# Kernel tuning notes

Hardware: AMD Instinct MI355X
Metric: run time of the kernel (lower is better)

The kernel has to match this reference:

```python
import jax, jax.numpy as jnp
import numpy as np

SEGMENT_LENGTHS = [2048, 4096]
DILATION_RATES = [1, 2]


def _group_attention(qg, kg, vg, seg_len, r, gidx):
    # qg/kg/vg: [b, gh, n, d]; segmented dilated attention for one head group.
    b, gh, n, d = qg.shape
    nseg = n // seg_len
    scale = float(1.0 / np.sqrt(d))
    qs = qg.reshape(b, gh, nseg, seg_len, d)
    ks = kg.reshape(b, gh, nseg, seg_len, d)
    vs = vg.reshape(b, gh, nseg, seg_len, d)
    if r > 1:
        m = seg_len // r
        # offset = (group_idx + seg_idx) % r; pattern = offset + r*arange(m) (no wrap since seg_len % r == 0)
        offsets = (gidx + jnp.arange(nseg)) % r            # [nseg]
        idx = offsets[:, None] + r * jnp.arange(m)[None, :]  # [nseg, m]
        si = jnp.arange(nseg)[:, None]                      # [nseg, 1]
        qd = qs[:, :, si, idx]                              # [b, gh, nseg, m, d]
        kd = ks[:, :, si, idx]
        vd = vs[:, :, si, idx]
    else:
        qd, kd, vd = qs, ks, vs
    scores = jnp.einsum('bgsqd,bgskd->bgsqk', qd, kd) * scale
    attn = jax.nn.softmax(scores, axis=-1)
    out = jnp.einsum('bgsqk,bgskd->bgsqd', attn, vd)
    if r > 1:
        # scatter dilated outputs back to their segment positions; unselected positions stay 0
        full = jnp.zeros((b, gh, nseg, seg_len, d), dtype=qg.dtype)
        out = full.at[:, :, si, idx].set(out)
    return out.reshape(b, gh, n, d)


def reference(q, k, v):
    # q, k, v: [b, n, h, d]; ring_size == 1 -> single-device dilated attention
    b, n, h, d = q.shape
    ngroups = len(SEGMENT_LENGTHS)
    gsize = h // ngroups
    qt = jnp.transpose(q, (0, 2, 1, 3))  # [b, h, n, d]
    kt = jnp.transpose(k, (0, 2, 1, 3))
    vt = jnp.transpose(v, (0, 2, 1, 3))
    outs = []
    for i, (s, r) in enumerate(zip(SEGMENT_LENGTHS, DILATION_RATES)):
        hs, he = i * gsize, (i + 1) * gsize
        outs.append(_group_attention(qt[:, hs:he], kt[:, hs:he], vt[:, hs:he], s, r, i))
    out = jnp.concatenate(outs, axis=1)   # [b, h, n, d]
    return jnp.transpose(out, (0, 2, 1, 3))  # [b, n, h, d]


def setup_inputs() -> dict:
    key = jax.random.key(0)
    kq, kk, kv = jax.random.split(key, 3)
    shape = (1, 8192, 16, 128)
    return {
        'q': jax.random.normal(kq, shape, dtype=jnp.float32),
        'k': jax.random.normal(kk, shape, dtype=jnp.float32),
        'v': jax.random.normal(kv, shape, dtype=jnp.float32),
    }
```

## Files before the change

### kernel.cpp

```cpp
#include <hip/hip_runtime.h>
#include <hip/hip_bf16.h>

typedef __attribute__((ext_vector_type(8)))  short bf16x8;
typedef __attribute__((ext_vector_type(4)))  float f32x4;
typedef __attribute__((ext_vector_type(16))) float f32x16;
typedef __attribute__((ext_vector_type(4)))  int   int4v;

__device__ __forceinline__ short f2bf(float f) {
    unsigned u = __builtin_bit_cast(unsigned, f);
    unsigned r = u + 0x7fffu + ((u >> 16) & 1u);
    return (short)(r >> 16);
}

__device__ __forceinline__ int row_map(int p, int j) {
    if (p < 32) return (p & 3) * 2048 + j;
    return ((p - 32) & 1) == 0 ? (2 * j + 1) : (4096 + 2 * j);
}
__device__ __forceinline__ int head_of(int p) {
    return (p < 32) ? (p >> 2) : (8 + ((p - 32) >> 1));
}

#define GLDS(gsrc, ldst)                                                          \
    __builtin_amdgcn_global_load_lds(                                             \
        (const __attribute__((address_space(1))) unsigned int*)(gsrc),            \
        (__attribute__((address_space(3))) unsigned int*)(ldst), 16, 0, 0)

__global__ __launch_bounds__(256) void conv_k_kernel(
    const float* __restrict__ K, short* __restrict__ Kws)
{
    const int cid = blockIdx.x * 256 + threadIdx.x;
    const int p   = cid >> 15;
    const int rem = cid & 32767;
    const int row = rem >> 4;
    const int d8  = (rem & 15) << 3;
    const int g   = row_map(p, row);
    const float* src = K + ((size_t)(g * 16 + head_of(p))) * 128 + d8;
    bf16x8 o;
    #pragma unroll
    for (int e = 0; e < 8; ++e) o[e] = f2bf(src[e]);
    *(bf16x8*)(Kws + (((size_t)p * 2048 + row) << 7) + d8) = o;
}

__global__ __launch_bounds__(256) void conv_v_kernel(
    const float* __restrict__ V, short* __restrict__ Vws)
{
    __shared__ short T[128][72];
    const int p  = blockIdx.x >> 5;
    const int kb = blockIdx.x & 31;
    const int tid = threadIdx.x;
    const int h = head_of(p);
    #pragma unroll
    for (int it = 0; it < 4; ++it) {
        const int cid  = it * 256 + tid;
        const int krow = cid & 63;
        const int d8   = (cid >> 6) << 3;
        const int g = row_map(p, kb * 64 + krow);
        const float* vp = V + ((size_t)(g * 16 + h)) * 128 + d8;
        #pragma unroll
        for (int e = 0; e < 8; ++e) T[d8 + e][krow] = f2bf(vp[e]);
    }
    __syncthreads();
    #pragma unroll
    for (int it = 0; it < 4; ++it) {
        const int j   = it * 256 + tid;
        const int d   = j >> 3;
        const int c16 = j & 7;
        bf16x8 val = *(const bf16x8*)&T[d][c16 * 8];
        *(bf16x8*)(Vws + ((size_t)p * 128 + d) * 2048 + kb * 64 + c16 * 8) = val;
    }
}

__global__ __launch_bounds__(256, 2) void dilated_attn5_kernel(
    const float* __restrict__ Q, const short* __restrict__ Kws,
    const short* __restrict__ Vws, float* __restrict__ O)
{
    __shared__ short Ks[2][64 * 128];
    __shared__ short Vt[2][128 * 64];
    __shared__ float sbuf[4][32];

    const int logical = (blockIdx.x & 7) * 96 + (blockIdx.x >> 3);
    const int pid  = logical >> 4;
    const int tile = logical & 15;
    const int h    = head_of(pid);

    const int tid  = threadIdx.x;
    const int wave = tid >> 6;
    const int lane = tid & 63;
    const int ql   = lane & 31;
    const int hi   = lane >> 5;

    const float scale_log2e = 0.08838834764831845f * 1.4426950408889634f;

    const short* Kp = Kws + ((size_t)pid * 2048 << 7);
    const short* Vp = Vws + ((size_t)pid * 128) * 2048;

    bf16x8 qf[8];
    {
        const int j = tile * 128 + wave * 32 + ql;
        const int g = row_map(pid, j);
        const float* qp = Q + ((size_t)(g * 16 + h)) * 128 + hi * 8;
        #pragma unroll
        for (int c = 0; c < 8; ++c) {
            bf16x8 f;
            #pragma unroll
            for (int e = 0; e < 8; ++e) f[e] = f2bf(qp[c * 16 + e] * scale_log2e);
            qf[c] = f;
        }
    }

    f32x16 oacc[4];
    #pragma unroll
    for (int dt = 0; dt < 4; ++dt) oacc[dt] = (f32x16)0.f;
    float m = -3.0e38f, l = 0.f;

    auto STAGE = [&](int buf, int kb) {
        #pragma unroll
        for (int it = 0; it < 4; ++it) {
            const int j   = it * 256 + wave * 64 + lane;
            const int row = j >> 4;
            const int u   = j & 15;
            GLDS(Kp + (((size_t)(kb * 64 + row)) << 7) + ((u ^ (row & 15)) << 3),
                 &Ks[buf][(it * 256 + wave * 64) * 8]);
        }
        #pragma unroll
        for (int it = 0; it < 4; ++it) {
            const int j   = it * 256 + wave * 64 + lane;
            const int row = j >> 3;
            const int u   = j & 7;
            GLDS(Vp + (size_t)row * 2048 + kb * 64 + ((u ^ (row & 7)) << 3),
                 &Vt[buf][(it * 256 + wave * 64) * 8]);
        }
    };

    STAGE(0, 0);
    asm volatile("s_waitcnt vmcnt(0)" ::: "memory");
    __syncthreads();

    for (int kb = 0; kb < 32; ++kb) {
        const int cur = kb & 1;
        if (kb + 1 < 32) STAGE(cur ^ 1, kb + 1);

        f32x16 p[2];
        __builtin_amdgcn_s_setprio(1);
        #pragma unroll
        for (int kt2 = 0; kt2 < 2; ++kt2) {
            f32x16 acc = (f32x16)0.f;
            const int row = kt2 * 32 + ql;
            #pragma unroll
            for (int c = 0; c < 8; ++c) {
                const int u = 2 * c + hi;
                bf16x8 a = *(const bf16x8*)&Ks[cur][row * 128 + ((u ^ (row & 15)) << 3)];
                acc = __builtin_amdgcn_mfma_f32_32x32x16_bf16(a, qf[c], acc, 0, 0, 0);
            }
            p[kt2] = acc;
        }
        __builtin_amdgcn_s_setprio(0);

        float rm = p[0][0];
        #pragma unroll
        for (int kt2 = 0; kt2 < 2; ++kt2)
            #pragma unroll
            for (int r = 0; r < 16; ++r) rm = fmaxf(rm, p[kt2][r]);
        rm = fmaxf(rm, __shfl_xor(rm, 32));

        if (__any(rm > m + 8.0f)) {
            const float mn = fmaxf(m, rm);
            const float sf = exp2f(m - mn);
            m = mn;
            l *= sf;
            if (lane < 32) sbuf[wave][lane] = sf;
            #pragma unroll
            for (int r = 0; r < 16; ++r) {
                const float s = sbuf[wave][(r & 3) + 8 * (r >> 2) + 4 * hi];
                #pragma unroll
                for (int dt = 0; dt < 4; ++dt) oacc[dt][r] *= s;
            }
        }

        float rs = 0.f;
        #pragma unroll
        for (int kt2 = 0; kt2 < 2; ++kt2)
            #pragma unroll
            for (int r = 0; r < 16; ++r) {
                const float pv = exp2f(p[kt2][r] - m);
                p[kt2][r] = pv;
                rs += pv;
            }
        rs += __shfl_xor(rs, 32);
        l += rs;

        bf16x8 pa[4];
        #pragma unroll
        for (int kt2 = 0; kt2 < 2; ++kt2) {
            int A0, A1, B0, B1, C0, C1, D0, D1;
            asm("v_cvt_pk_bf16_f32 %0,%1,%2" : "=v"(A0) : "v"(p[kt2][0]),  "v"(p[kt2][1]));
            asm("v_cvt_pk_bf16_f32 %0,%1,%2" : "=v"(A1) : "v"(p[kt2][2]),  "v"(p[kt2][3]));
            asm("v_cvt_pk_bf16_f32 %0,%1,%2" : "=v"(B0) : "v"(p[kt2][4]),  "v"(p[kt2][5]));
            asm("v_cvt_pk_bf16_f32 %0,%1,%2" : "=v"(B1) : "v"(p[kt2][6]),  "v"(p[kt2][7]));
            asm("v_cvt_pk_bf16_f32 %0,%1,%2" : "=v"(C0) : "v"(p[kt2][8]),  "v"(p[kt2][9]));
            asm("v_cvt_pk_bf16_f32 %0,%1,%2" : "=v"(C1) : "v"(p[kt2][10]), "v"(p[kt2][11]));
            asm("v_cvt_pk_bf16_f32 %0,%1,%2" : "=v"(D0) : "v"(p[kt2][12]), "v"(p[kt2][13]));
            asm("v_cvt_pk_bf16_f32 %0,%1,%2" : "=v"(D1) : "v"(p[kt2][14]), "v"(p[kt2][15]));
            asm("v_permlane32_swap_b32 %0, %1" : "+v"(A0), "+v"(B0));
            asm("v_permlane32_swap_b32 %0, %1" : "+v"(A1), "+v"(B1));
            asm("v_permlane32_swap_b32 %0, %1" : "+v"(C0), "+v"(D0));
            asm("v_permlane32_swap_b32 %0, %1" : "+v"(C1), "+v"(D1));
            pa[2 * kt2 + 0] = __builtin_bit_cast(bf16x8, (int4v){A0, A1, B0, B1});
            pa[2 * kt2 + 1] = __builtin_bit_cast(bf16x8, (int4v){C0, C1, D0, D1});
        }

        __builtin_amdgcn_s_setprio(1);
        #pragma unroll
        for (int ks = 0; ks < 4; ++ks) {
            #pragma unroll
            for (int dt = 0; dt < 4; ++dt) {
                const int row = dt * 32 + ql;
                const int u   = 2 * ks + hi;
                bf16x8 vb = *(const bf16x8*)&Vt[cur][row * 64 + ((u ^ (row & 7)) << 3)];
                oacc[dt] = __builtin_amdgcn_mfma_f32_32x32x16_bf16(pa[ks], vb, oacc[dt], 0, 0, 0);
            }
        }
        __builtin_amdgcn_s_setprio(0);

        asm volatile("s_waitcnt vmcnt(0)" ::: "memory");
        __syncthreads();
    }

    if (lane < 32) sbuf[wave][lane] = 1.f / l;
    #pragma unroll
    for (int r = 0; r < 16; ++r) {
        const int qrow = (r & 3) + 8 * (r >> 2) + 4 * hi;
        const float inv = sbuf[wave][qrow];
        const int j = tile * 128 + wave * 32 + qrow;
        const int g = row_map(pid, j);
        float* op = O + ((size_t)(g * 16 + h)) * 128 + ql;
        #pragma unroll
        for (int dt = 0; dt < 4; ++dt)
            op[dt * 32] = oacc[dt][r] * inv;
    }
}

__global__ __launch_bounds__(256) void zero_fill_kernel(float* __restrict__ O)
{
    const int t = blockIdx.x * 256 + threadIdx.x;
    const int c4   = t & 31;
    const int rowi = (t >> 5) & 4095;
    const int hh   = t >> 17;
    const int row  = (rowi < 2048) ? (2 * rowi) : (4096 + 2 * (rowi - 2048) + 1);
    float4 z; z.x = 0.f; z.y = 0.f; z.z = 0.f; z.w = 0.f;
    *(float4*)&O[((size_t)(row * 16) + 8 + hh) * 128 + c4 * 4] = z;
}

#define BK    64
#define KPAD  136
#define VPAD  72
__global__ __launch_bounds__(256) void dilated_attn_v1_kernel(
    const float* __restrict__ Q, const float* __restrict__ K,
    const float* __restrict__ V, float* __restrict__ O)
{
    __shared__ short KsL[BK][KPAD];
    __shared__ short VtL[128][VPAD];
    __shared__ short PsL[4][16][VPAD];
    const int bid  = blockIdx.x;
    const int p    = bid >> 5;
    const int tile = bid & 31;
    const int h    = head_of(p);
    const int tid  = threadIdx.x;
    const int wave = tid >> 6;
    const int lane = tid & 63;
    const int lr   = lane & 15;
    const int lg   = lane >> 4;
    const float scale_log2e = 0.08838834764831845f * 1.4426950408889634f;
    bf16x8 qf[4];
    {
        const int j = tile * 64 + wave * 16 + lr;
        const int g = row_map(p, j);
        const float* qp = Q + ((size_t)(g * 16 + h)) * 128 + lg * 8;
        #pragma unroll
        for (int c = 0; c < 4; ++c) {
            bf16x8 f;
            #pragma unroll
            for (int e = 0; e < 8; ++e) f[e] = f2bf(qp[c * 32 + e] * scale_log2e);
            qf[c] = f;
        }
    }
    f32x4 oacc[8];
    #pragma unroll
    for (int i = 0; i < 8; ++i) oacc[i] = (f32x4)0.f;
    float m[4], l[4];
    #pragma unroll
    for (int r = 0; r < 4; ++r) { m[r] = -3.0e38f; l[r] = 0.f; }
    for (int kb = 0; kb < 2048 / BK; ++kb) {
        __syncthreads();
        #pragma unroll
        for (int it = 0; it < 4; ++it) {
            const int cid  = it * 256 + tid;
            const int krow = cid >> 4;
            const int dcol = (cid & 15) << 3;
            const int g = row_map(p, kb * BK + krow);
            const float* kp = K + ((size_t)(g * 16 + h)) * 128 + dcol;
            bf16x8 kk;
            #pragma unroll
            for (int e = 0; e < 8; ++e) kk[e] = f2bf(kp[e]);
            *(bf16x8*)&KsL[krow][dcol] = kk;
        }
        #pragma unroll
        for (int it = 0; it < 4; ++it) {
            const int cid  = it * 256 + tid;
            const int krow = cid & 63;
            const int dcol = (cid >> 6) << 3;
            const int g = row_map(p, kb * BK + krow);
            const float* vp = V + ((size_t)(g * 16 + h)) * 128 + dcol;
            #pragma unroll
            for (int e = 0; e < 8; ++e) VtL[dcol + e][krow] = f2bf(vp[e]);
        }
        __syncthreads();
        f32x4 s[4];
        #pragma unroll
        for (int t = 0; t < 4; ++t) {
            f32x4 acc = (f32x4)0.f;
            #pragma unroll
            for (int c = 0; c < 4; ++c) {
                bf16x8 b = *(const bf16x8*)&KsL[t * 16 + lr][c * 32 + lg * 8];
                acc = __builtin_amdgcn_mfma_f32_16x16x32_bf16(qf[c], b, acc, 0, 0, 0);
            }
            s[t] = acc;
        }
        #pragma unroll
        for (int r = 0; r < 4; ++r) {
            float bm = fmaxf(fmaxf(s[0][r], s[1][r]), fmaxf(s[2][r], s[3][r]));
            bm = fmaxf(bm, __shfl_xor(bm, 1));
            bm = fmaxf(bm, __shfl_xor(bm, 2));
            bm = fmaxf(bm, __shfl_xor(bm, 4));
            bm = fmaxf(bm, __shfl_xor(bm, 8));
            const float mn = fmaxf(m[r], bm);
            const float sf = exp2f(m[r] - mn);
            m[r] = mn;
            float rs = 0.f;
            #pragma unroll
            for (int t = 0; t < 4; ++t) {
                const float pv = exp2f(s[t][r] - mn);
                s[t][r] = pv;
                rs += pv;
            }
            rs += __shfl_xor(rs, 1);
            rs += __shfl_xor(rs, 2);
            rs += __shfl_xor(rs, 4);
            rs += __shfl_xor(rs, 8);
            l[r] = l[r] * sf + rs;
            #pragma unroll
            for (int dt = 0; dt < 8; ++dt) oacc[dt][r] *= sf;
        }
        #pragma unroll
        for (int t = 0; t < 4; ++t)
            #pragma unroll
            for (int r = 0; r < 4; ++r)
                PsL[wave][lg * 4 + r][t * 16 + lr] = f2bf(s[t][r]);
        #pragma unroll
        for (int cc = 0; cc < 2; ++cc) {
            bf16x8 pa = *(const bf16x8*)&PsL[wave][lr][cc * 32 + lg * 8];
            #pragma unroll
            for (int dt = 0; dt < 8; ++dt) {
                bf16x8 vb = *(const bf16x8*)&VtL[dt * 16 + lr][cc * 32 + lg * 8];
                oacc[dt] = __builtin_amdgcn_mfma_f32_16x16x32_bf16(pa, vb, oacc[dt], 0, 0, 0);
            }
        }
    }
    #pragma unroll
    for (int r = 0; r < 4; ++r) {
        const int j = tile * 64 + wave * 16 + lg * 4 + r;
        const int g = row_map(p, j);
        const float inv = 1.f / l[r];
        float* op = O + ((size_t)(g * 16 + h)) * 128 + lr;
        #pragma unroll
        for (int dt = 0; dt < 8; ++dt)
            op[dt * 16] = oacc[dt][r] * inv;
    }
}

extern "C" void kernel_launch(void* const* d_in, const int* in_sizes, int n_in,
                              void* d_out, int out_size, void* d_ws, size_t ws_size,
                              hipStream_t stream) {
    const float* q = (const float*)d_in[0];
    const float* k = (const float*)d_in[1];
    const float* v = (const float*)d_in[2];
    float* o = (float*)d_out;

    const size_t kws_elems = (size_t)48 * 2048 * 128;
    const size_t need = kws_elems * 2 * 2;
    hipLaunchKernelGGL(zero_fill_kernel, dim3(4096), dim3(256), 0, stream, o);
    if (ws_size >= need) {
        short* kws = (short*)d_ws;
        short* vws = kws + kws_elems;
        hipLaunchKernelGGL(conv_k_kernel, dim3(6144), dim3(256), 0, stream, k, kws);
        hipLaunchKernelGGL(conv_v_kernel, dim3(1536), dim3(256), 0, stream, v, vws);
        hipLaunchKernelGGL(dilated_attn5_kernel, dim3(48 * 16), dim3(256), 0, stream,
                           q, kws, vws, o);
    } else {
        hipLaunchKernelGGL(dilated_attn_v1_kernel, dim3(48 * 32), dim3(256), 0, stream,
                           q, k, v, o);
    }
}
```

Measured before the change: 195.2 us.

## Process two query sub-tiles per wave with triple-buffered 32-row KV staging

Each wave now handles 64 query rows as two 32-row groups that share every K and V fragment read from LDS, so LDS traffic per MFMA is halved. The block tile grows to 256 queries, which halves the grid to 384 blocks. KV blocks shrink to 32 keys and move to a three-stage ring with a partial vmcnt wait, letting loads run two steps ahead. The cost is double the accumulator and Q-fragment registers, which may limit occupancy, and fewer blocks than the machine has CUs.

```diff
diff --git a/kernel.cpp b/kernel.cpp
--- a/kernel.cpp
+++ b/kernel.cpp
@@ -70,17 +70,17 @@
     }
 }
 
-__global__ __launch_bounds__(256, 2) void dilated_attn5_kernel(
+__global__ __launch_bounds__(256, 2) void dilated_attn6_kernel(
     const float* __restrict__ Q, const short* __restrict__ Kws,
     const short* __restrict__ Vws, float* __restrict__ O)
 {
-    __shared__ short Ks[2][64 * 128];
-    __shared__ short Vt[2][128 * 64];
-    __shared__ float sbuf[4][32];
-
-    const int logical = (blockIdx.x & 7) * 96 + (blockIdx.x >> 3);
-    const int pid  = logical >> 4;
-    const int tile = logical & 15;
+    __shared__ short Ks[3][32 * 128];
+    __shared__ short Vt[3][128 * 32];
+    __shared__ float sbuf[4][64];
+
+    const int logical = (blockIdx.x & 7) * 48 + (blockIdx.x >> 3);
+    const int pid  = logical >> 3;
+    const int tile = logical & 7;
     const int h    = head_of(pid);
 
     const int tid  = threadIdx.x;
@@ -94,149 +94,202 @@
     const short* Kp = Kws + ((size_t)pid * 2048 << 7);
     const short* Vp = Vws + ((size_t)pid * 128) * 2048;
 
-    bf16x8 qf[8];
+    bf16x8 qfA[8], qfB[8];
     {
-        const int j = tile * 128 + wave * 32 + ql;
-        const int g = row_map(pid, j);
-        const float* qp = Q + ((size_t)(g * 16 + h)) * 128 + hi * 8;
+        const int jA = tile * 256 + wave * 64 + ql;
+        const int gA = row_map(pid, jA);
+        const float* qpA = Q + ((size_t)(gA * 16 + h)) * 128 + hi * 8;
+        const int gB = row_map(pid, jA + 32);
+        const float* qpB = Q + ((size_t)(gB * 16 + h)) * 128 + hi * 8;
         #pragma unroll
         for (int c = 0; c < 8; ++c) {
-            bf16x8 f;
-            #pragma unroll
-            for (int e = 0; e < 8; ++e) f[e] = f2bf(qp[c * 16 + e] * scale_log2e);
-            qf[c] = f;
-        }
-    }
-
-    f32x16 oacc[4];
-    #pragma unroll
-    for (int dt = 0; dt < 4; ++dt) oacc[dt] = (f32x16)0.f;
-    float m = -3.0e38f, l = 0.f;
+            bf16x8 fa, fb;
+            #pragma unroll
+            for (int e = 0; e < 8; ++e) {
+                fa[e] = f2bf(qpA[c * 16 + e] * scale_log2e);
+                fb[e] = f2bf(qpB[c * 16 + e] * scale_log2e);
+            }
+            qfA[c] = fa; qfB[c] = fb;
+        }
+    }
+
+    f32x16 oaccA[4], oaccB[4];
+    #pragma unroll
+    for (int dt = 0; dt < 4; ++dt) { oaccA[dt] = (f32x16)0.f; oaccB[dt] = (f32x16)0.f; }
+    float mA = -3.0e38f, lA = 0.f, mB = -3.0e38f, lB = 0.f;
 
     auto STAGE = [&](int buf, int kb) {
         #pragma unroll
-        for (int it = 0; it < 4; ++it) {
+        for (int it = 0; it < 2; ++it) {
             const int j   = it * 256 + wave * 64 + lane;
             const int row = j >> 4;
             const int u   = j & 15;
-            GLDS(Kp + (((size_t)(kb * 64 + row)) << 7) + ((u ^ (row & 15)) << 3),
+            GLDS(Kp + (((size_t)(kb * 32 + row)) << 7) + ((u ^ (row & 15)) << 3),
                  &Ks[buf][(it * 256 + wave * 64) * 8]);
         }
         #pragma unroll
-        for (int it = 0; it < 4; ++it) {
+        for (int it = 0; it < 2; ++it) {
             const int j   = it * 256 + wave * 64 + lane;
-            const int row = j >> 3;
-            const int u   = j & 7;
-            GLDS(Vp + (size_t)row * 2048 + kb * 64 + ((u ^ (row & 7)) << 3),
+            const int row = j >> 2;
+            const int u   = j & 3;
+            GLDS(Vp + (size_t)row * 2048 + kb * 32 + ((u ^ ((row >> 1) & 3)) << 3),
                  &Vt[buf][(it * 256 + wave * 64) * 8]);
         }
     };
 
     STAGE(0, 0);
-    asm volatile("s_waitcnt vmcnt(0)" ::: "memory");
+    STAGE(1, 1);
+    asm volatile("s_waitcnt vmcnt(4)" ::: "memory");
     __syncthreads();
 
-    for (int kb = 0; kb < 32; ++kb) {
-        const int cur = kb & 1;
-        if (kb + 1 < 32) STAGE(cur ^ 1, kb + 1);
-
-        f32x16 p[2];
+    int cur = 0, nxt2 = 2;
+    for (int t = 0; t < 64; ++t) {
+        if (t < 62) STAGE(nxt2, t + 2);
+
+        f32x16 pA = (f32x16)0.f, pB = (f32x16)0.f;
         __builtin_amdgcn_s_setprio(1);
         #pragma unroll
-        for (int kt2 = 0; kt2 < 2; ++kt2) {
-            f32x16 acc = (f32x16)0.f;
-            const int row = kt2 * 32 + ql;
-            #pragma unroll
-            for (int c = 0; c < 8; ++c) {
-                const int u = 2 * c + hi;
-                bf16x8 a = *(const bf16x8*)&Ks[cur][row * 128 + ((u ^ (row & 15)) << 3)];
-                acc = __builtin_amdgcn_mfma_f32_32x32x16_bf16(a, qf[c], acc, 0, 0, 0);
-            }
-            p[kt2] = acc;
+        for (int c = 0; c < 8; ++c) {
+            const bf16x8 kf = *(const bf16x8*)
+                &Ks[cur][(ql * 16 + ((2 * c + hi) ^ (ql & 15))) * 8];
+            pA = __builtin_amdgcn_mfma_f32_32x32x16_bf16(kf, qfA[c], pA, 0, 0, 0);
+            pB = __builtin_amdgcn_mfma_f32_32x32x16_bf16(kf, qfB[c], pB, 0, 0, 0);
         }
         __builtin_amdgcn_s_setprio(0);
 
-        float rm = p[0][0];
-        #pragma unroll
-        for (int kt2 = 0; kt2 < 2; ++kt2)
-            #pragma unroll
-            for (int r = 0; r < 16; ++r) rm = fmaxf(rm, p[kt2][r]);
-        rm = fmaxf(rm, __shfl_xor(rm, 32));
-
-        if (__any(rm > m + 8.0f)) {
-            const float mn = fmaxf(m, rm);
-            const float sf = exp2f(m - mn);
-            m = mn;
-            l *= sf;
-            if (lane < 32) sbuf[wave][lane] = sf;
+        {
+            float rm = pA[0];
+            #pragma unroll
+            for (int r = 1; r < 16; ++r) rm = fmaxf(rm, pA[r]);
+            rm = fmaxf(rm, __shfl_xor(rm, 32));
+            if (__any(rm > mA + 8.0f)) {
+                const float mn = fmaxf(mA, rm);
+                const float sf = exp2f(mA - mn);
+                mA = mn; lA *= sf;
+                if (lane < 32) sbuf[wave][lane] = sf;
+                #pragma unroll
+                for (int r = 0; r < 16; ++r) {
+                    const float s = sbuf[wave][(r & 3) + 8 * (r >> 2) + 4 * hi];
+                    #pragma unroll
+                    for (int dt = 0; dt < 4; ++dt) oaccA[dt][r] *= s;
+                }
+            }
+            float rs = 0.f;
             #pragma unroll
             for (int r = 0; r < 16; ++r) {
-                const float s = sbuf[wave][(r & 3) + 8 * (r >> 2) + 4 * hi];
+                const float pv = exp2f(pA[r] - mA);
+                pA[r] = pv; rs += pv;
+            }
+            rs += __shfl_xor(rs, 32);
+            lA += rs;
+        }
+        {
+            float rm = pB[0];
+            #pragma unroll
+            for (int r = 1; r < 16; ++r) rm = fmaxf(rm, pB[r]);
+            rm = fmaxf(rm, __shfl_xor(rm, 32));
+            if (__any(rm > mB + 8.0f)) {
+                const float mn = fmaxf(mB, rm);
+                const float sf = exp2f(mB - mn);
+                mB = mn; lB *= sf;
+                if (lane < 32) sbuf[wave][32 + lane] = sf;
                 #pragma unroll
-                for (int dt = 0; dt < 4; ++dt) oacc[dt][r] *= s;
-            }
-        }
-
-        float rs = 0.f;
-        #pragma unroll
-        for (int kt2 = 0; kt2 < 2; ++kt2)
+                for (int r = 0; r < 16; ++r) {
+                    const float s = sbuf[wave][32 + (r & 3) + 8 * (r >> 2) + 4 * hi];
+                    #pragma unroll
+                    for (int dt = 0; dt < 4; ++dt) oaccB[dt][r] *= s;
+                }
+            }
+            float rs = 0.f;
             #pragma unroll
             for (int r = 0; r < 16; ++r) {
-                const float pv = exp2f(p[kt2][r] - m);
-                p[kt2][r] = pv;
-                rs += pv;
-            }
-        rs += __shfl_xor(rs, 32);
-        l += rs;
-
-        bf16x8 pa[4];
-        #pragma unroll
-        for (int kt2 = 0; kt2 < 2; ++kt2) {
+                const float pv = exp2f(pB[r] - mB);
+                pB[r] = pv; rs += pv;
+            }
+            rs += __shfl_xor(rs, 32);
+            lB += rs;
+        }
+
+        bf16x8 paA[2], paB[2];
+        {
             int A0, A1, B0, B1, C0, C1, D0, D1;
-            asm("v_cvt_pk_bf16_f32 %0,%1,%2" : "=v"(A0) : "v"(p[kt2][0]),  "v"(p[kt2][1]));
-            asm("v_cvt_pk_bf16_f32 %0,%1,%2" : "=v"(A1) : "v"(p[kt2][2]),  "v"(p[kt2][3]));
-            asm("v_cvt_pk_bf16_f32 %0,%1,%2" : "=v"(B0) : "v"(p[kt2][4]),  "v"(p[kt2][5]));
-            asm("v_cvt_pk_bf16_f32 %0,%1,%2" : "=v"(B1) : "v"(p[kt2][6]),  "v"(p[kt2][7]));
-            asm("v_cvt_pk_bf16_f32 %0,%1,%2" : "=v"(C0) : "v"(p[kt2][8]),  "v"(p[kt2][9]));
-            asm("v_cvt_pk_bf16_f32 %0,%1,%2" : "=v"(C1) : "v"(p[kt2][10]), "v"(p[kt2][11]));
-            asm("v_cvt_pk_bf16_f32 %0,%1,%2" : "=v"(D0) : "v"(p[kt2][12]), "v"(p[kt2][13]));
-            asm("v_cvt_pk_bf16_f32 %0,%1,%2" : "=v"(D1) : "v"(p[kt2][14]), "v"(p[kt2][15]));
+            asm("v_cvt_pk_bf16_f32 %0,%1,%2" : "=v"(A0) : "v"(pA[0]),  "v"(pA[1]));
+            asm("v_cvt_pk_bf16_f32 %0,%1,%2" : "=v"(A1) : "v"(pA[2]),  "v"(pA[3]));
+            asm("v_cvt_pk_bf16_f32 %0,%1,%2" : "=v"(B0) : "v"(pA[4]),  "v"(pA[5]));
+            asm("v_cvt_pk_bf16_f32 %0,%1,%2" : "=v"(B1) : "v"(pA[6]),  "v"(pA[7]));
+            asm("v_cvt_pk_bf16_f32 %0,%1,%2" : "=v"(C0) : "v"(pA[8]),  "v"(pA[9]));
+            asm("v_cvt_pk_bf16_f32 %0,%1,%2" : "=v"(C1) : "v"(pA[10]), "v"(pA[11]));
+            asm("v_cvt_pk_bf16_f32 %0,%1,%2" : "=v"(D0) : "v"(pA[12]), "v"(pA[13]));
+            asm("v_cvt_pk_bf16_f32 %0,%1,%2" : "=v"(D1) : "v"(pA[14]), "v"(pA[15]));
             asm("v_permlane32_swap_b32 %0, %1" : "+v"(A0), "+v"(B0));
             asm("v_permlane32_swap_b32 %0, %1" : "+v"(A1), "+v"(B1));
             asm("v_permlane32_swap_b32 %0, %1" : "+v"(C0), "+v"(D0));
             asm("v_permlane32_swap_b32 %0, %1" : "+v"(C1), "+v"(D1));
-            pa[2 * kt2 + 0] = __builtin_bit_cast(bf16x8, (int4v){A0, A1, B0, B1});
-            pa[2 * kt2 + 1] = __builtin_bit_cast(bf16x8, (int4v){C0, C1, D0, D1});
+            paA[0] = __builtin_bit_cast(bf16x8, (int4v){A0, A1, B0, B1});
+            paA[1] = __builtin_bit_cast(bf16x8, (int4v){C0, C1, D0, D1});
+        }
+        {
+            int A0, A1, B0, B1, C0, C1, D0, D1;
+            asm("v_cvt_pk_bf16_f32 %0,%1,%2" : "=v"(A0) : "v"(pB[0]),  "v"(pB[1]));
+            asm("v_cvt_pk_bf16_f32 %0,%1,%2" : "=v"(A1) : "v"(pB[2]),  "v"(pB[3]));
+            asm("v_cvt_pk_bf16_f32 %0,%1,%2" : "=v"(B0) : "v"(pB[4]),  "v"(pB[5]));
+            asm("v_cvt_pk_bf16_f32 %0,%1,%2" : "=v"(B1) : "v"(pB[6]),  "v"(pB[7]));
+            asm("v_cvt_pk_bf16_f32 %0,%1,%2" : "=v"(C0) : "v"(pB[8]),  "v"(pB[9]));
+            asm("v_cvt_pk_bf16_f32 %0,%1,%2" : "=v"(C1) : "v"(pB[10]), "v"(pB[11]));
+            asm("v_cvt_pk_bf16_f32 %0,%1,%2" : "=v"(D0) : "v"(pB[12]), "v"(pB[13]));
+            asm("v_cvt_pk_bf16_f32 %0,%1,%2" : "=v"(D1) : "v"(pB[14]), "v"(pB[15]));
+            asm("v_permlane32_swap_b32 %0, %1" : "+v"(A0), "+v"(B0));
+            asm("v_permlane32_swap_b32 %0, %1" : "+v"(A1), "+v"(B1));
+            asm("v_permlane32_swap_b32 %0, %1" : "+v"(C0), "+v"(D0));
+            asm("v_permlane32_swap_b32 %0, %1" : "+v"(C1), "+v"(D1));
+            paB[0] = __builtin_bit_cast(bf16x8, (int4v){A0, A1, B0, B1});
+            paB[1] = __builtin_bit_cast(bf16x8, (int4v){C0, C1, D0, D1});
         }
 
         __builtin_amdgcn_s_setprio(1);
         #pragma unroll
-        for (int ks = 0; ks < 4; ++ks) {
+        for (int ks = 0; ks < 2; ++ks) {
             #pragma unroll
             for (int dt = 0; dt < 4; ++dt) {
                 const int row = dt * 32 + ql;
-                const int u   = 2 * ks + hi;
-                bf16x8 vb = *(const bf16x8*)&Vt[cur][row * 64 + ((u ^ (row & 7)) << 3)];
-                oacc[dt] = __builtin_amdgcn_mfma_f32_32x32x16_bf16(pa[ks], vb, oacc[dt], 0, 0, 0);
+                const bf16x8 vb = *(const bf16x8*)
+                    &Vt[cur][(row * 4 + ((ks * 2 + hi) ^ ((row >> 1) & 3))) * 8];
+                oaccA[dt] = __builtin_amdgcn_mfma_f32_32x32x16_bf16(paA[ks], vb, oaccA[dt], 0, 0, 0);
+                oaccB[dt] = __builtin_amdgcn_mfma_f32_32x32x16_bf16(paB[ks], vb, oaccB[dt], 0, 0, 0);
             }
         }
         __builtin_amdgcn_s_setprio(0);
 
-        asm volatile("s_waitcnt vmcnt(0)" ::: "memory");
+        if (t < 62) asm volatile("s_waitcnt vmcnt(4)" ::: "memory");
+        else        asm volatile("s_waitcnt vmcnt(0)" ::: "memory");
         __syncthreads();
-    }
-
-    if (lane < 32) sbuf[wave][lane] = 1.f / l;
+
+        cur  = (cur == 2)  ? 0 : cur + 1;
+        nxt2 = (nxt2 == 2) ? 0 : nxt2 + 1;
+    }
+
+    if (lane < 32) { sbuf[wave][lane] = 1.f / lA; sbuf[wave][32 + lane] = 1.f / lB; }
     #pragma unroll
     for (int r = 0; r < 16; ++r) {
         const int qrow = (r & 3) + 8 * (r >> 2) + 4 * hi;
-        const float inv = sbuf[wave][qrow];
-        const int j = tile * 128 + wave * 32 + qrow;
-        const int g = row_map(pid, j);
-        float* op = O + ((size_t)(g * 16 + h)) * 128 + ql;
-        #pragma unroll
-        for (int dt = 0; dt < 4; ++dt)
-            op[dt * 32] = oacc[dt][r] * inv;
+        {
+            const float inv = sbuf[wave][qrow];
+            const int j = tile * 256 + wave * 64 + qrow;
+            const int g = row_map(pid, j);
+            float* op = O + ((size_t)(g * 16 + h)) * 128 + ql;
+            #pragma unroll
+            for (int dt = 0; dt < 4; ++dt)
+                op[dt * 32] = oaccA[dt][r] * inv;
+        }
+        {
+            const float inv = sbuf[wave][32 + qrow];
+            const int j = tile * 256 + wave * 64 + 32 + qrow;
+            const int g = row_map(pid, j);
+            float* op = O + ((size_t)(g * 16 + h)) * 128 + ql;
+            #pragma unroll
+            for (int dt = 0; dt < 4; ++dt)
+                op[dt * 32] = oaccB[dt][r] * inv;
+        }
     }
 }
 
@@ -394,7 +447,7 @@
         short* vws = kws + kws_elems;
         hipLaunchKernelGGL(conv_k_kernel, dim3(6144), dim3(256), 0, stream, k, kws);
         hipLaunchKernelGGL(conv_v_kernel, dim3(1536), dim3(256), 0, stream, v, vws);
-        hipLaunchKernelGGL(dilated_attn5_kernel, dim3(48 * 16), dim3(256), 0, stream,
+        hipLaunchKernelGGL(dilated_attn6_kernel, dim3(48 * 8), dim3(256), 0, stream,
                            q, kws, vws, o);
     } else {
         hipLaunchKernelGGL(dilated_attn_v1_kernel, dim3(48 * 32), dim3(256), 0, stream,
```

Result: slower. 251.4 us (+28.8%).
